# Optimization experiments

Hardware: AMD Instinct MI355X
Metric: run time of the kernel (lower is better)

## Reference

```python
import jax, jax.numpy as jnp
import numpy as np

B, T, H, NH = 4, 1024, 1024, 16
HS = H // NH
FF = 4 * H
EPS = 1e-5


def setup_inputs() -> dict:
    key = jax.random.key(0)
    ks = jax.random.split(key, 12)
    s = 0.02
    inp = {
        "x": jax.random.normal(ks[0], (B, T, H), jnp.float32),
        # attention projections, stored as [in, out] so y = x @ W + b
        "Wq": jax.random.normal(ks[1], (H, H), jnp.float32) * s,
        "bq": jnp.zeros((H,), jnp.float32),
        "Wk": jax.random.normal(ks[2], (H, H), jnp.float32) * s,
        "bk": jnp.zeros((H,), jnp.float32),
        "Wv": jax.random.normal(ks[3], (H, H), jnp.float32) * s,
        "bv": jnp.zeros((H,), jnp.float32),
        "Wo": jax.random.normal(ks[4], (H, H), jnp.float32) * s,
        "bo": jnp.zeros((H,), jnp.float32),
        # layernorms
        "ln1_w": jnp.ones((H,), jnp.float32),
        "ln1_b": jnp.zeros((H,), jnp.float32),
        "ln2_w": jnp.ones((H,), jnp.float32),
        "ln2_b": jnp.zeros((H,), jnp.float32),
        # MLP
        "Wfc": jax.random.normal(ks[5], (H, FF), jnp.float32) * s,
        "bfc": jnp.zeros((FF,), jnp.float32),
        "Wpr": jax.random.normal(ks[6], (FF, H), jnp.float32) * s,
        "bpr": jnp.zeros((H,), jnp.float32),
    }
    return inp


def _layernorm(x, w, b):
    mu = jnp.mean(x, axis=-1, keepdims=True)
    var = jnp.mean(jnp.square(x - mu), axis=-1, keepdims=True)
    return (x - mu) * jax.lax.rsqrt(var + EPS) * w + b


def _rope(x):
    # x: [B, nh, T, hs]; interleaved-pair RoPE, base 10000
    half = HS // 2
    inv_freq = 1.0 / (10000.0 ** (jnp.arange(half, dtype=jnp.float32) / half))
    ang = jnp.arange(T, dtype=jnp.float32)[:, None] * inv_freq[None, :]  # [T, half]
    cos, sin = jnp.cos(ang), jnp.sin(ang)
    xr = x.reshape(*x.shape[:-1], half, 2)
    x0, x1 = xr[..., 0], xr[..., 1]
    r0 = x0 * cos - x1 * sin
    r1 = x0 * sin + x1 * cos
    return jnp.stack([r0, r1], axis=-1).reshape(x.shape)


def _block(x, Wq, bq, Wk, bk, Wv, bv, Wo, bo, ln1_w, ln1_b, ln2_w, ln2_b, Wfc, bfc, Wpr, bpr):
    # --- attention sub-block ---
    h1 = _layernorm(x, ln1_w, ln1_b)
    q = (h1 @ Wq + bq).reshape(B, T, NH, HS).transpose(0, 2, 1, 3)  # [B,nh,T,hs]
    k = (h1 @ Wk + bk).reshape(B, T, NH, HS).transpose(0, 2, 1, 3)
    v = (h1 @ Wv + bv).reshape(B, T, NH, HS).transpose(0, 2, 1, 3)
    q, k = _rope(q), _rope(k)
    scores = jnp.einsum('bhqd,bhkd->bhqk', q, k) / jnp.sqrt(jnp.float32(HS))
    attn = jax.nn.softmax(scores, axis=-1)
    # NOTE: original applies the causal mask AFTER softmax (multiplicative, no renorm)
    causal = jnp.tril(jnp.ones((T, T), jnp.float32))[None, None]
    attn = attn * causal
    out = jnp.einsum('bhqk,bhkd->bhqd', attn, v)
    out = out.transpose(0, 2, 1, 3).reshape(B, T, H)
    x = x + (out @ Wo + bo)
    # --- MLP sub-block ---
    h2 = _layernorm(x, ln2_w, ln2_b)
    m = jax.nn.gelu(h2 @ Wfc + bfc, approximate=False)
    x = x + (m @ Wpr + bpr)
    return x


def reference(x, Wq, bq, Wk, bk, Wv, bv, Wo, bo, ln1_w, ln1_b, ln2_w, ln2_b, Wfc, bfc, Wpr, bpr):
    return _block(x, Wq, bq, Wk, bk, Wv, bv, Wo, bo, ln1_w, ln1_b, ln2_w, ln2_b, Wfc, bfc, Wpr, bpr)
```

## Files before the change

kernel.cpp:

```cpp
#include <hip/hip_runtime.h>
#include <hip/hip_bf16.h>

typedef unsigned short u16;
typedef __attribute__((ext_vector_type(8))) short bf16x8;
typedef __attribute__((ext_vector_type(4))) float f32x4;
typedef __attribute__((ext_vector_type(4))) unsigned short u16x4;

#define B_  4
#define T_  1024
#define H_  1024
#define NH_ 16
#define HS_ 64
#define FF_ 4096
#define M_  (B_*T_)
#define QKV_S 3072

__device__ __forceinline__ u16 f2bf(float f){
  union { float f; unsigned u; } v; v.f = f;
  unsigned r = v.u + 0x7fffu + ((v.u >> 16) & 1u);
  return (u16)(r >> 16);
}
__device__ __forceinline__ float bf2f(u16 h){
  union { unsigned u; float f; } v; v.u = ((unsigned)h) << 16;
  return v.f;
}
__device__ __forceinline__ unsigned pack2bf(float a, float b){
  __hip_bfloat162 h = __float22bfloat162_rn(make_float2(a, b));
  union { __hip_bfloat162 h; unsigned u; } c; c.h = h;
  return c.u;
}

__device__ __forceinline__ void gload_lds16(const void* g, void* l){
  __builtin_amdgcn_global_load_lds(
      (const __attribute__((address_space(1))) unsigned int*)g,
      (__attribute__((address_space(3))) unsigned int*)l,
      16, 0, 0);
}

__global__ __launch_bounds__(256) void transpose_cvt(const float* __restrict__ W,
                                                     u16* __restrict__ Wt, int K, int N)
{
  __shared__ u16 tile[64][68];
  const int k0 = blockIdx.y * 64, n0 = blockIdx.x * 64;
  const int tid = threadIdx.x;
  #pragma unroll
  for (int it = 0; it < 4; ++it){
    int ci = tid + it * 256;
    int kr = ci >> 4, nc = ci & 15;
    float4 f = *(const float4*)(W + (size_t)(k0 + kr) * N + n0 + nc * 4);
    tile[kr][nc*4+0] = f2bf(f.x);
    tile[kr][nc*4+1] = f2bf(f.y);
    tile[kr][nc*4+2] = f2bf(f.z);
    tile[kr][nc*4+3] = f2bf(f.w);
  }
  __syncthreads();
  #pragma unroll
  for (int it = 0; it < 4; ++it){
    int co = tid + it * 256;
    int nr = co >> 4, kc = co & 15;
    u16x4 o;
    o[0] = tile[kc*4+0][nr];
    o[1] = tile[kc*4+1][nr];
    o[2] = tile[kc*4+2][nr];
    o[3] = tile[kc*4+3][nr];
    *(u16x4*)(Wt + (size_t)(n0 + nr) * K + k0 + kc * 4) = o;
  }
}

__global__ __launch_bounds__(256) void vtrans_k(const u16* __restrict__ qkv,
                                                u16* __restrict__ vtg)
{
  __shared__ u16 tile[64][72];
  const int bh = blockIdx.y, tt = blockIdx.x * 64;
  const int b = bh >> 4, h = bh & 15;
  const size_t src = (size_t)b * T_ * QKV_S + h * HS_ + 2048;
  const int tid = threadIdx.x;
  #pragma unroll
  for (int it = 0; it < 2; ++it){
    int ci = tid + it * 256;
    int r = ci >> 3, c = ci & 7;
    bf16x8 vvv = *(const bf16x8*)(qkv + src + (size_t)(tt + r) * QKV_S + c * 8);
    *(bf16x8*)&tile[r][c * 8] = vvv;
  }
  __syncthreads();
  #pragma unroll
  for (int it = 0; it < 2; ++it){
    int co = tid + it * 256;
    int d = co >> 3, c = co & 7;
    bf16x8 ov;
    #pragma unroll
    for (int j = 0; j < 8; ++j) ov[j] = (short)tile[c * 8 + j][d];
    *(bf16x8*)(vtg + (size_t)bh * HS_ * T_ + (size_t)d * T_ + tt + c * 8) = ov;
  }
}

__global__ void concat3_k(const float* __restrict__ a, const float* __restrict__ b,
                          const float* __restrict__ c, float* __restrict__ o){
  int i = blockIdx.x * 256 + threadIdx.x;
  if (i >= QKV_S) return;
  o[i] = (i < 1024) ? a[i] : (i < 2048) ? b[i - 1024] : c[i - 2048];
}

__global__ void rope_table_k(float* __restrict__ tab){
  int i = blockIdx.x * blockDim.x + threadIdx.x;
  if (i >= T_ * 32) return;
  int t = i >> 5, f = i & 31;
  float inv = powf(10000.0f, -(float)f * (1.0f / 32.0f));
  float ang = (float)t * inv;
  tab[i*2+0] = cosf(ang);
  tab[i*2+1] = sinf(ang);
}

__global__ void rope_apply_k(u16* __restrict__ qkv, const float* __restrict__ tab){
  int i = blockIdx.x * blockDim.x + threadIdx.x;
  if (i >= B_*T_*NH_*32) return;
  int pr = i & 31;
  int nh = (i >> 5) & (NH_ - 1);
  int bt = i >> 9;
  int t  = bt & (T_ - 1);
  size_t idx = (size_t)bt * QKV_S + nh * HS_ + pr * 2;
  float c = tab[(t*32 + pr)*2], s = tab[(t*32 + pr)*2 + 1];
  {
    float x0 = bf2f(qkv[idx]), x1 = bf2f(qkv[idx+1]);
    qkv[idx]   = f2bf((x0 * c - x1 * s) * 0.125f);
    qkv[idx+1] = f2bf((x0 * s + x1 * c) * 0.125f);
  }
  {
    float x0 = bf2f(qkv[idx+1024]), x1 = bf2f(qkv[idx+1025]);
    qkv[idx+1024] = f2bf(x0 * c - x1 * s);
    qkv[idx+1025] = f2bf(x0 * s + x1 * c);
  }
}

__global__ __launch_bounds__(256) void ln_kernel(const float* __restrict__ x,
    const float* __restrict__ w, const float* __restrict__ bgain,
    u16* __restrict__ out)
{
  const int row = blockIdx.x;
  const int t = threadIdx.x;
  float4 vv = ((const float4*)(x + (size_t)row * H_))[t];
  float s  = vv.x + vv.y + vv.z + vv.w;
  float s2 = vv.x*vv.x + vv.y*vv.y + vv.z*vv.z + vv.w*vv.w;
  #pragma unroll
  for (int mm = 1; mm < 64; mm <<= 1){ s += __shfl_xor(s, mm); s2 += __shfl_xor(s2, mm); }
  __shared__ float red[8];
  int wid = t >> 6;
  if ((t & 63) == 0){ red[wid] = s; red[4 + wid] = s2; }
  __syncthreads();
  s  = red[0] + red[1] + red[2] + red[3];
  s2 = red[4] + red[5] + red[6] + red[7];
  float mu  = s * (1.0f / H_);
  float var = s2 * (1.0f / H_) - mu * mu;
  float rin = rsqrtf(var + 1e-5f);
  float4 wv = ((const float4*)w)[t];
  float4 bv = ((const float4*)bgain)[t];
  u16x4 ov;
  ov[0] = f2bf((vv.x - mu) * rin * wv.x + bv.x);
  ov[1] = f2bf((vv.y - mu) * rin * wv.y + bv.y);
  ov[2] = f2bf((vv.z - mu) * rin * wv.z + bv.z);
  ov[3] = f2bf((vv.w - mu) * rin * wv.w + bv.w);
  ((u16x4*)(out + (size_t)row * H_))[t] = ov;
}

template<int EPI, int RING>
__global__ __launch_bounds__(512) void gemm_kernel(
    const u16* __restrict__ A, const u16* __restrict__ Bt,
    const float* __restrict__ bias, const float* __restrict__ res,
    void* __restrict__ Cout, int M, int N, int K)
{
  __shared__ __attribute__((aligned(16))) u16 As[RING][128 * 32];
  __shared__ __attribute__((aligned(16))) u16 Bs[RING][128 * 32];
  const int tid  = threadIdx.x;
  const int lane = tid & 63;
  const int wid  = tid >> 6;
  const int wm = wid >> 2, wn = wid & 3;
  const int lrow = lane & 15, lkg = lane >> 4;

  const int gx  = gridDim.x;
  const int nwg = gx * gridDim.y;
  const int wg  = blockIdx.y * gx + blockIdx.x;
  const int nx  = nwg >> 3;
  const int swz = (wg & 7) * nx + (wg >> 3);
  const int m0 = (swz / gx) * 128, n0 = (swz % gx) * 128;

  const int srow = tid >> 2;
  const int sdc  = tid & 3;
  const int scs  = sdc ^ ((srow >> 1) & 3);

  const u16* Arow = A  + (size_t)(m0 + srow) * K + scs * 8;
  const u16* Brow = Bt + (size_t)(n0 + srow) * K + scs * 8;
  const int dd = (srow * 4 + sdc) * 8;

  f32x4 acc[4][2] = {};
  const int NT = K >> 5;
  constexpr int DIST = RING - 1;

  #pragma unroll
  for (int s = 0; s < DIST; ++s){
    gload_lds16(Arow + (s << 5), &As[s][dd]);
    gload_lds16(Brow + (s << 5), &Bs[s][dd]);
  }

  int rs = 0, wsl = DIST;
  for (int t = 0; t < NT; ++t){
    int cnt = NT - 1 - t; if (cnt > DIST - 1) cnt = DIST - 1;
    if (cnt >= 4)      asm volatile("s_waitcnt vmcnt(8)" ::: "memory");
    else if (cnt == 3) asm volatile("s_waitcnt vmcnt(6)" ::: "memory");
    else if (cnt == 2) asm volatile("s_waitcnt vmcnt(4)" ::: "memory");
    else if (cnt == 1) asm volatile("s_waitcnt vmcnt(2)" ::: "memory");
    else               asm volatile("s_waitcnt vmcnt(0)" ::: "memory");
    __builtin_amdgcn_s_barrier();

    const u16* Asc = As[rs];
    const u16* Bsc = Bs[rs];
    rs = (rs + 1 == RING) ? 0 : rs + 1;

    bf16x8 af[4], bfr[2];
    #pragma unroll
    for (int mi = 0; mi < 4; ++mi){
      int r = wm*64 + mi*16 + lrow;
      af[mi] = *(const bf16x8*)&Asc[(r*4 + (lkg ^ ((r >> 1) & 3))) * 8];
    }
    #pragma unroll
    for (int ni = 0; ni < 2; ++ni){
      int r = wn*32 + ni*16 + lrow;
      bfr[ni] = *(const bf16x8*)&Bsc[(r*4 + (lkg ^ ((r >> 1) & 3))) * 8];
    }
    __builtin_amdgcn_sched_barrier(0);

    if (t + DIST < NT){
      int k0 = (t + DIST) << 5;
      gload_lds16(Arow + k0, &As[wsl][dd]);
      gload_lds16(Brow + k0, &Bs[wsl][dd]);
    }
    wsl = (wsl + 1 == RING) ? 0 : wsl + 1;

    #pragma unroll
    for (int mi = 0; mi < 4; ++mi)
      #pragma unroll
      for (int ni = 0; ni < 2; ++ni)
        acc[mi][ni] = __builtin_amdgcn_mfma_f32_16x16x32_bf16(af[mi], bfr[ni], acc[mi][ni], 0, 0, 0);
  }

  #pragma unroll
  for (int mi = 0; mi < 4; ++mi){
    #pragma unroll
    for (int ni = 0; ni < 2; ++ni){
      int col = n0 + wn*32 + ni*16 + lrow;
      float bv = bias[col];
      #pragma unroll
      for (int r = 0; r < 4; ++r){
        int row = m0 + wm*64 + mi*16 + lkg*4 + r;
        float v = acc[mi][ni][r] + bv;
        if (EPI == 1){
          v = 0.5f * v * (1.0f + erff(v * 0.70710678118f));
        }
        if (EPI == 2){
          ((float*)Cout)[(size_t)row * N + col] = v + res[(size_t)row * N + col];
        } else {
          ((u16*)Cout)[(size_t)row * N + col] = f2bf(v);
        }
      }
    }
  }
}

__global__ __launch_bounds__(256) void attn_kernel(
    const u16* __restrict__ qkv, const u16* __restrict__ vtg,
    u16* __restrict__ out)
{
  __shared__ u16 K_lds[3][64 * 64];
  __shared__ u16 VT_lds[3][64 * 64];
  __shared__ u16 P_lds[4][16 * 64];
  const int tid = threadIdx.x, lane = tid & 63, w = tid >> 6;
  const int lrow = lane & 15, lkg = lane >> 4;
  const int q0 = blockIdx.x * 64;
  const int bh = blockIdx.y, b = bh >> 4, h = bh & 15;
  const size_t baseq  = (size_t)b * T_ * QKV_S + h * HS_;
  const size_t basek  = baseq + 1024;
  const size_t basevt = (size_t)bh * HS_ * T_;
  const size_t baseo  = (size_t)b * T_ * H_ + h * HS_;
  const int qg = q0 + w * 16 + lrow;

  bf16x8 qa[2];
  {
    const u16* qp = qkv + baseq + (size_t)qg * QKV_S + lkg * 8;
    qa[0] = *(const bf16x8*)qp;
    qa[1] = *(const bf16x8*)(qp + 32);
  }

  const int ci0 = tid, ci1 = tid + 256;
  const int r0 = ci0 >> 3, c0 = ci0 & 7, g0 = c0 ^ (r0 & 7);
  const int r1 = ci1 >> 3, c1 = ci1 & 7, g1 = c1 ^ (r1 & 7);
  const u16* kap0 = qkv + basek + (size_t)r0 * QKV_S + g0 * 8;
  const u16* kap1 = qkv + basek + (size_t)r1 * QKV_S + g1 * 8;
  const u16* vap0 = vtg + basevt + (size_t)r0 * T_ + g0 * 8;
  const u16* vap1 = vtg + basevt + (size_t)r1 * T_ + g1 * 8;
  const int kd0 = ci0 * 8, kd1 = ci1 * 8;

  f32x4 o[4] = {};
  float mrun = -1e30f, lrun = 0.f;

  #pragma unroll
  for (int s = 0; s < 2; ++s){
    const size_t ko = (size_t)s * 64 * QKV_S;
    const int    vo = s * 64;
    gload_lds16(kap0 + ko, &K_lds[s][kd0]);
    gload_lds16(kap1 + ko, &K_lds[s][kd1]);
    gload_lds16(vap0 + vo, &VT_lds[s][kd0]);
    gload_lds16(vap1 + vo, &VT_lds[s][kd1]);
  }

  int rs = 0, wsl = 2;
  for (int t = 0; t < 16; ++t){
    const int kt = t << 6;
    if (t < 15) asm volatile("s_waitcnt vmcnt(4)" ::: "memory");
    else        asm volatile("s_waitcnt vmcnt(0)" ::: "memory");
    __builtin_amdgcn_s_barrier();
    __builtin_amdgcn_sched_barrier(0);

    if (t + 2 < 16){
      const size_t ko = (size_t)(t + 2) * 64 * QKV_S;
      const int    vo = (t + 2) * 64;
      gload_lds16(kap0 + ko, &K_lds[wsl][kd0]);
      gload_lds16(kap1 + ko, &K_lds[wsl][kd1]);
      gload_lds16(vap0 + vo, &VT_lds[wsl][kd0]);
      gload_lds16(vap1 + vo, &VT_lds[wsl][kd1]);
    }
    wsl = (wsl + 1 == 3) ? 0 : wsl + 1;

    const u16* Kc  = K_lds[rs];
    const u16* VTc = VT_lds[rs];
    rs = (rs + 1 == 3) ? 0 : rs + 1;

    f32x4 s[4];
    #pragma unroll
    for (int mi = 0; mi < 4; ++mi){
      f32x4 c = {};
      #pragma unroll
      for (int ss = 0; ss < 2; ++ss){
        int r = mi * 16 + lrow;
        int off = r * 128 + (((ss * 4 + lkg) ^ (r & 7)) * 16);
        bf16x8 kb = *(const bf16x8*)((const char*)Kc + off);
        c = __builtin_amdgcn_mfma_f32_16x16x32_bf16(kb, qa[ss], c, 0, 0, 0);
      }
      s[mi] = c;
    }

    float mt = fmaxf(fmaxf(fmaxf(s[0][0], s[0][1]), fmaxf(s[0][2], s[0][3])),
                     fmaxf(fmaxf(s[1][0], s[1][1]), fmaxf(s[1][2], s[1][3])));
    mt = fmaxf(mt, fmaxf(fmaxf(fmaxf(s[2][0], s[2][1]), fmaxf(s[2][2], s[2][3])),
                         fmaxf(fmaxf(s[3][0], s[3][1]), fmaxf(s[3][2], s[3][3]))));
    mt = fmaxf(mt, __shfl_xor(mt, 16));
    mt = fmaxf(mt, __shfl_xor(mt, 32));
    float mnew = fmaxf(mrun, mt);
    float fsc = __expf(mrun - mnew);
    mrun = mnew;

    float p[16];
    float ls = 0.f;
    #pragma unroll
    for (int mi = 0; mi < 4; ++mi){
      #pragma unroll
      for (int r = 0; r < 4; ++r){
        int key = kt + mi * 16 + lkg * 4 + r;
        float pv = __expf(s[mi][r] - mnew);
        ls += pv;
        p[mi * 4 + r] = (key <= qg) ? pv : 0.f;
      }
    }
    ls += __shfl_xor(ls, 16);
    ls += __shfl_xor(ls, 32);
    lrun = lrun * fsc + ls;
    #pragma unroll
    for (int nf = 0; nf < 4; ++nf){
      #pragma unroll
      for (int r = 0; r < 4; ++r) o[nf][r] *= fsc;
    }

    if (kt <= q0 + w * 16 + 15){
      char* pbase = (char*)&P_lds[w][0];
      const int rx = (lrow & 7) << 4;
      #pragma unroll
      for (int mi = 0; mi < 4; ++mi){
        uint2 pk;
        pk.x = pack2bf(p[mi*4+0], p[mi*4+1]);
        pk.y = pack2bf(p[mi*4+2], p[mi*4+3]);
        *(uint2*)(pbase + (lrow * 128 + ((mi * 32 + lkg * 8) ^ rx))) = pk;
      }
      #pragma unroll
      for (int ss = 0; ss < 2; ++ss){
        bf16x8 pb = *(const bf16x8*)(pbase + (lrow * 128 + ((ss * 64 + lkg * 16) ^ rx)));
        #pragma unroll
        for (int nfd = 0; nfd < 4; ++nfd){
          int d = nfd * 16 + lrow;
          int off = d * 128 + (((ss * 4 + lkg) ^ (d & 7)) * 16);
          bf16x8 vb = *(const bf16x8*)((const char*)VTc + off);
          o[nfd] = __builtin_amdgcn_mfma_f32_16x16x32_bf16(vb, pb, o[nfd], 0, 0, 0);
        }
      }
    }
  }

  float rl = 1.0f / lrun;
  #pragma unroll
  for (int nfd = 0; nfd < 4; ++nfd){
    uint2 ov;
    ov.x = pack2bf(o[nfd][0] * rl, o[nfd][1] * rl);
    ov.y = pack2bf(o[nfd][2] * rl, o[nfd][3] * rl);
    *(uint2*)(out + baseo + (size_t)qg * H_ + nfd * 16 + lkg * 4) = ov;
  }
}

extern "C" void kernel_launch(void* const* d_in, const int* in_sizes, int n_in,
                              void* d_out, int out_size, void* d_ws, size_t ws_size,
                              hipStream_t stream)
{
  (void)in_sizes; (void)n_in; (void)out_size; (void)ws_size;
  const float* x    = (const float*)d_in[0];
  const float* Wq   = (const float*)d_in[1];
  const float* bq   = (const float*)d_in[2];
  const float* Wk   = (const float*)d_in[3];
  const float* bk   = (const float*)d_in[4];
  const float* Wv   = (const float*)d_in[5];
  const float* bv   = (const float*)d_in[6];
  const float* Wo   = (const float*)d_in[7];
  const float* bo   = (const float*)d_in[8];
  const float* ln1w = (const float*)d_in[9];
  const float* ln1b = (const float*)d_in[10];
  const float* ln2w = (const float*)d_in[11];
  const float* ln2b = (const float*)d_in[12];
  const float* Wfc  = (const float*)d_in[13];
  const float* bfc  = (const float*)d_in[14];
  const float* Wpr  = (const float*)d_in[15];
  const float* bpr  = (const float*)d_in[16];

  char* ws = (char*)d_ws;
  u16*  WqkvT = (u16*)(ws + ((size_t) 0 << 20));
  u16*  WoT   = (u16*)(ws + ((size_t) 6 << 20));
  u16*  WfcT  = (u16*)(ws + ((size_t) 8 << 20));
  u16*  WprT  = (u16*)(ws + ((size_t)16 << 20));
  u16*  h1    = (u16*)(ws + ((size_t)24 << 20));
  u16*  qkvb  = (u16*)(ws + ((size_t)32 << 20));
  float* x1   = (float*)(ws + ((size_t)32 << 20));
  u16*  h2    = (u16*)(ws + ((size_t)48 << 20));
  float* bqkv = (float*)(ws + ((size_t)56 << 20));
  float* rtab = (float*)(ws + ((size_t)56 << 20) + (64 << 10));
  u16*  vtg   = (u16*)(ws + ((size_t)57 << 20));
  u16*  mb    = (u16*)(ws + ((size_t)56 << 20));
  u16*  attnout = h1;

  dim3 blk(256);
  dim3 gblk(512);

  transpose_cvt<<<dim3(H_/64,  H_/64),  blk, 0, stream>>>(Wq,  WqkvT,                 H_,  H_);
  transpose_cvt<<<dim3(H_/64,  H_/64),  blk, 0, stream>>>(Wk,  WqkvT + (size_t)1024*1024, H_,  H_);
  transpose_cvt<<<dim3(H_/64,  H_/64),  blk, 0, stream>>>(Wv,  WqkvT + (size_t)2048*1024, H_,  H_);
  transpose_cvt<<<dim3(H_/64,  H_/64),  blk, 0, stream>>>(Wo,  WoT,  H_,  H_);
  transpose_cvt<<<dim3(FF_/64, H_/64),  blk, 0, stream>>>(Wfc, WfcT, H_,  FF_);
  transpose_cvt<<<dim3(H_/64,  FF_/64), blk, 0, stream>>>(Wpr, WprT, FF_, H_);
  concat3_k<<<dim3((QKV_S+255)/256), blk, 0, stream>>>(bq, bk, bv, bqkv);
  rope_table_k<<<dim3((T_*32)/256), blk, 0, stream>>>(rtab);

  ln_kernel<<<dim3(M_), blk, 0, stream>>>(x, ln1w, ln1b, h1);
  gemm_kernel<0,3><<<dim3(QKV_S/128, M_/128), gblk, 0, stream>>>(h1, WqkvT, bqkv, nullptr, qkvb, M_, QKV_S, H_);
  rope_apply_k<<<dim3((B_*T_*NH_*32)/256), blk, 0, stream>>>(qkvb, rtab);
  vtrans_k<<<dim3(T_/64, B_*NH_), blk, 0, stream>>>(qkvb, vtg);
  attn_kernel<<<dim3(T_/64, B_*NH_), blk, 0, stream>>>(qkvb, vtg, attnout);
  gemm_kernel<2,6><<<dim3(H_/128, M_/128), gblk, 0, stream>>>(attnout, WoT, bo, x, x1, M_, H_, H_);
  ln_kernel<<<dim3(M_), blk, 0, stream>>>(x1, ln2w, ln2b, h2);
  gemm_kernel<1,3><<<dim3(FF_/128, M_/128), gblk, 0, stream>>>(h2, WfcT, bfc, nullptr, mb, M_, FF_, H_);
  gemm_kernel<2,6><<<dim3(H_/128, M_/128), gblk, 0, stream>>>(mb, WprT, bpr, x1, (float*)d_out, M_, H_, FF_);
}
```

Baseline: 267.5 us.

## Widen attention blocks to 128 queries, lazy rescale softmax in base-2, set MFMA priority

The attention kernel now runs 512 threads per block covering 128 queries, so each K/V tile staged in LDS is shared by eight waves instead of four and each thread issues half as many async loads. Q is pre-scaled by log2(e) during RoPE so the softmax can use exp2f. The running max and rescale of O and l only happen when some lane's new max exceeds the old one by more than 8, so most tiles skip the rescale multiplies. s_setprio is raised around the MFMA sections. The risks are bf16 overflow headroom from the lazy max, since values up to 2^8 can accumulate before a rescale, and fewer blocks in the grid (512 instead of 1024) for the scheduler to spread across CUs.

New measurement: 263.3 us. No clear change (-1.6%).

```diff
diff --git a/kernel.cpp b/kernel.cpp
--- a/kernel.cpp
+++ b/kernel.cpp
@@ -120,10 +120,11 @@
   int t  = bt & (T_ - 1);
   size_t idx = (size_t)bt * QKV_S + nh * HS_ + pr * 2;
   float c = tab[(t*32 + pr)*2], s = tab[(t*32 + pr)*2 + 1];
+  const float qs = 0.125f * 1.44269504f;
   {
     float x0 = bf2f(qkv[idx]), x1 = bf2f(qkv[idx+1]);
-    qkv[idx]   = f2bf((x0 * c - x1 * s) * 0.125f);
-    qkv[idx+1] = f2bf((x0 * s + x1 * c) * 0.125f);
+    qkv[idx]   = f2bf((x0 * c - x1 * s) * qs);
+    qkv[idx+1] = f2bf((x0 * s + x1 * c) * qs);
   }
   {
     float x0 = bf2f(qkv[idx+1024]), x1 = bf2f(qkv[idx+1025]);
@@ -265,16 +266,16 @@
   }
 }
 
-__global__ __launch_bounds__(256) void attn_kernel(
+__global__ __launch_bounds__(512, 4) void attn_kernel(
     const u16* __restrict__ qkv, const u16* __restrict__ vtg,
     u16* __restrict__ out)
 {
   __shared__ u16 K_lds[3][64 * 64];
   __shared__ u16 VT_lds[3][64 * 64];
-  __shared__ u16 P_lds[4][16 * 64];
+  __shared__ u16 P_lds[8][16 * 64];
   const int tid = threadIdx.x, lane = tid & 63, w = tid >> 6;
   const int lrow = lane & 15, lkg = lane >> 4;
-  const int q0 = blockIdx.x * 64;
+  const int q0 = blockIdx.x * 128;
   const int bh = blockIdx.y, b = bh >> 4, h = bh & 15;
   const size_t baseq  = (size_t)b * T_ * QKV_S + h * HS_;
   const size_t basek  = baseq + 1024;
@@ -289,43 +290,31 @@
     qa[1] = *(const bf16x8*)(qp + 32);
   }
 
-  const int ci0 = tid, ci1 = tid + 256;
-  const int r0 = ci0 >> 3, c0 = ci0 & 7, g0 = c0 ^ (r0 & 7);
-  const int r1 = ci1 >> 3, c1 = ci1 & 7, g1 = c1 ^ (r1 & 7);
-  const u16* kap0 = qkv + basek + (size_t)r0 * QKV_S + g0 * 8;
-  const u16* kap1 = qkv + basek + (size_t)r1 * QKV_S + g1 * 8;
-  const u16* vap0 = vtg + basevt + (size_t)r0 * T_ + g0 * 8;
-  const u16* vap1 = vtg + basevt + (size_t)r1 * T_ + g1 * 8;
-  const int kd0 = ci0 * 8, kd1 = ci1 * 8;
+  const int r0 = tid >> 3, c0 = tid & 7, g0 = c0 ^ (r0 & 7);
+  const u16* kap = qkv + basek + (size_t)r0 * QKV_S + g0 * 8;
+  const u16* vap = vtg + basevt + (size_t)r0 * T_ + g0 * 8;
+  const int kd = tid * 8;
 
   f32x4 o[4] = {};
   float mrun = -1e30f, lrun = 0.f;
 
   #pragma unroll
   for (int s = 0; s < 2; ++s){
-    const size_t ko = (size_t)s * 64 * QKV_S;
-    const int    vo = s * 64;
-    gload_lds16(kap0 + ko, &K_lds[s][kd0]);
-    gload_lds16(kap1 + ko, &K_lds[s][kd1]);
-    gload_lds16(vap0 + vo, &VT_lds[s][kd0]);
-    gload_lds16(vap1 + vo, &VT_lds[s][kd1]);
+    gload_lds16(kap + (size_t)s * 64 * QKV_S, &K_lds[s][kd]);
+    gload_lds16(vap + s * 64,                 &VT_lds[s][kd]);
   }
 
   int rs = 0, wsl = 2;
   for (int t = 0; t < 16; ++t){
     const int kt = t << 6;
-    if (t < 15) asm volatile("s_waitcnt vmcnt(4)" ::: "memory");
+    if (t < 15) asm volatile("s_waitcnt vmcnt(2)" ::: "memory");
     else        asm volatile("s_waitcnt vmcnt(0)" ::: "memory");
     __builtin_amdgcn_s_barrier();
     __builtin_amdgcn_sched_barrier(0);
 
     if (t + 2 < 16){
-      const size_t ko = (size_t)(t + 2) * 64 * QKV_S;
-      const int    vo = (t + 2) * 64;
-      gload_lds16(kap0 + ko, &K_lds[wsl][kd0]);
-      gload_lds16(kap1 + ko, &K_lds[wsl][kd1]);
-      gload_lds16(vap0 + vo, &VT_lds[wsl][kd0]);
-      gload_lds16(vap1 + vo, &VT_lds[wsl][kd1]);
+      gload_lds16(kap + (size_t)(t + 2) * 64 * QKV_S, &K_lds[wsl][kd]);
+      gload_lds16(vap + (t + 2) * 64,                 &VT_lds[wsl][kd]);
     }
     wsl = (wsl + 1 == 3) ? 0 : wsl + 1;
 
@@ -334,6 +323,7 @@
     rs = (rs + 1 == 3) ? 0 : rs + 1;
 
     f32x4 s[4];
+    __builtin_amdgcn_s_setprio(1);
     #pragma unroll
     for (int mi = 0; mi < 4; ++mi){
       f32x4 c = {};
@@ -346,6 +336,7 @@
       }
       s[mi] = c;
     }
+    __builtin_amdgcn_s_setprio(0);
 
     float mt = fmaxf(fmaxf(fmaxf(s[0][0], s[0][1]), fmaxf(s[0][2], s[0][3])),
                      fmaxf(fmaxf(s[1][0], s[1][1]), fmaxf(s[1][2], s[1][3])));
@@ -353,9 +344,17 @@
                          fmaxf(fmaxf(s[3][0], s[3][1]), fmaxf(s[3][2], s[3][3]))));
     mt = fmaxf(mt, __shfl_xor(mt, 16));
     mt = fmaxf(mt, __shfl_xor(mt, 32));
-    float mnew = fmaxf(mrun, mt);
-    float fsc = __expf(mrun - mnew);
-    mrun = mnew;
+    if (!__all(mt <= mrun + 8.f)){
+      float mnew = fmaxf(mrun, mt);
+      float fsc = exp2f(mrun - mnew);
+      lrun *= fsc;
+      #pragma unroll
+      for (int nf = 0; nf < 4; ++nf){
+        #pragma unroll
+        for (int r = 0; r < 4; ++r) o[nf][r] *= fsc;
+      }
+      mrun = mnew;
+    }
 
     float p[16];
     float ls = 0.f;
@@ -364,19 +363,14 @@
       #pragma unroll
       for (int r = 0; r < 4; ++r){
         int key = kt + mi * 16 + lkg * 4 + r;
-        float pv = __expf(s[mi][r] - mnew);
+        float pv = exp2f(s[mi][r] - mrun);
         ls += pv;
         p[mi * 4 + r] = (key <= qg) ? pv : 0.f;
       }
     }
     ls += __shfl_xor(ls, 16);
     ls += __shfl_xor(ls, 32);
-    lrun = lrun * fsc + ls;
-    #pragma unroll
-    for (int nf = 0; nf < 4; ++nf){
-      #pragma unroll
-      for (int r = 0; r < 4; ++r) o[nf][r] *= fsc;
-    }
+    lrun += ls;
 
     if (kt <= q0 + w * 16 + 15){
       char* pbase = (char*)&P_lds[w][0];
@@ -388,6 +382,7 @@
         pk.y = pack2bf(p[mi*4+2], p[mi*4+3]);
         *(uint2*)(pbase + (lrow * 128 + ((mi * 32 + lkg * 8) ^ rx))) = pk;
       }
+      __builtin_amdgcn_s_setprio(1);
       #pragma unroll
       for (int ss = 0; ss < 2; ++ss){
         bf16x8 pb = *(const bf16x8*)(pbase + (lrow * 128 + ((ss * 64 + lkg * 16) ^ rx)));
@@ -399,6 +394,7 @@
           o[nfd] = __builtin_amdgcn_mfma_f32_16x16x32_bf16(vb, pb, o[nfd], 0, 0, 0);
         }
       }
+      __builtin_amdgcn_s_setprio(0);
     }
   }
 
@@ -466,7 +462,7 @@
   gemm_kernel<0,3><<<dim3(QKV_S/128, M_/128), gblk, 0, stream>>>(h1, WqkvT, bqkv, nullptr, qkvb, M_, QKV_S, H_);
   rope_apply_k<<<dim3((B_*T_*NH_*32)/256), blk, 0, stream>>>(qkvb, rtab);
   vtrans_k<<<dim3(T_/64, B_*NH_), blk, 0, stream>>>(qkvb, vtg);
-  attn_kernel<<<dim3(T_/64, B_*NH_), blk, 0, stream>>>(qkvb, vtg, attnout);
+  attn_kernel<<<dim3(T_/128, B_*NH_), dim3(512), 0, stream>>>(qkvb, vtg, attnout);
   gemm_kernel<2,6><<<dim3(H_/128, M_/128), gblk, 0, stream>>>(attnout, WoT, bo, x, x1, M_, H_, H_);
   ln_kernel<<<dim3(M_), blk, 0, stream>>>(x1, ln2w, ln2b, h2);
   gemm_kernel<1,3><<<dim3(FF_/128, M_/128), gblk, 0, stream>>>(h2, WfcT, bfc, nullptr, mb, M_, FF_, H_);
```
